# Optimization experiments

Measured on AMD Instinct MI355X. Metric: run time of the kernel, lower is better.

## Reference

```python
import jax, jax.numpy as jnp
import numpy as np

N, E, C, NB, NE, G = 20000, 320000, 64, 8, 4, 16
L2 = 9          # (max_ell+1)^2 with max_ell=2
RMAX = 5.0
HID = 16        # nonlinear readout hidden width


def setup_inputs():
    key = jax.random.key(0)
    ks = jax.random.split(key, 16)
    positions = jax.random.uniform(ks[0], (N, 3), dtype=jnp.float32) * 3.0
    elems = jax.random.randint(ks[1], (N,), 0, NE)
    node_attrs = jax.nn.one_hot(elems, NE, dtype=jnp.float32)
    edge_index = jax.random.randint(ks[2], (2, E), 0, N)
    batch = jnp.sort(jax.random.randint(ks[3], (N,), 0, G))
    shifts = jnp.zeros((E, 3), jnp.float32)
    atomic_energies = jnp.array([-1.0, -2.0, -3.0, -4.0], jnp.float32)
    sc = lambda k, shp, fan: jax.random.normal(k, shp, jnp.float32) / np.sqrt(fan).astype(np.float32)
    W_embed = sc(ks[4], (NE, C), NE)
    W_up = sc(ks[5], (2, C, C), C)
    W1 = sc(ks[6], (2, NB, 64), NB)
    W2 = sc(ks[7], (2, 64, C), 64)
    W_out = sc(ks[8], (2, C, C), C)
    W_skip = sc(ks[9], (2, NE, C), NE)
    w_read0 = sc(ks[10], (C,), C)
    W_r1 = sc(ks[11], (C, HID), C)
    w_r2 = sc(ks[12], (HID,), HID)
    return dict(positions=positions, node_attrs=node_attrs, shifts=shifts,
                atomic_energies=atomic_energies, W_embed=W_embed, W_up=W_up,
                W1=W1, W2=W2, W_out=W_out, W_skip=W_skip, w_read0=w_read0,
                W_r1=W_r1, w_r2=w_r2, edge_index=edge_index, batch=batch)


def _sph_harm_l2(u):
    # component-normalized real spherical harmonics up to l=2 on unit vectors
    x, y, z = u[:, 0], u[:, 1], u[:, 2]
    s3, s5, s15 = jnp.sqrt(3.0), jnp.sqrt(5.0), jnp.sqrt(15.0)
    return jnp.stack([jnp.ones_like(x),
                      s3 * x, s3 * y, s3 * z,
                      s15 * x * y, s15 * y * z, 0.5 * s5 * (3.0 * z * z - 1.0),
                      s15 * x * z, 0.5 * s15 * (x * x - y * y)], axis=-1)


def _radial(r):
    # Bessel radial basis with polynomial cutoff (p=6)
    n = jnp.arange(1, NB + 1, dtype=jnp.float32)
    rb = jnp.sqrt(2.0 / RMAX) * jnp.sin(n * jnp.pi * r[:, None] / RMAX) / r[:, None]
    u = r / RMAX
    fc = 1.0 - 28.0 * u**6 + 48.0 * u**7 - 21.0 * u**8
    fc = jnp.where(u < 1.0, fc, 0.0)
    return rb * fc[:, None]


def _energy_contributions(positions, node_attrs, shifts, atomic_energies,
                          W_embed, W_up, W1, W2, W_out, W_skip,
                          w_read0, W_r1, w_r2, edge_index, batch):
    snd, rcv = edge_index[0], edge_index[1]
    vec = positions[snd] - positions[rcv] + shifts                  # [E,3]
    r = jnp.sqrt(jnp.sum(vec * vec, axis=-1) + 1e-12)               # [E]
    Y = _sph_harm_l2(vec / r[:, None])                              # [E,L2]
    ef = _radial(r)                                                 # [E,NB]
    # E0: per-element reference energies, summed per graph
    e0 = jax.ops.segment_sum(node_attrs @ atomic_energies, batch, num_segments=G)
    h0 = node_attrs @ W_embed                                       # [N,C] scalar feats
    h = jnp.zeros((positions.shape[0], L2, C), h0.dtype).at[:, 0, :].set(h0)
    readouts = [lambda s: s @ w_read0,
                lambda s: jax.nn.silu(s @ W_r1) @ w_r2]             # linear / nonlinear
    energies = [e0]
    for i in range(2):
        hu = jnp.einsum('nlc,cd->nld', h, W_up[i])                  # channel mix
        R = jax.nn.silu(ef @ W1[i]) @ W2[i]                         # radial MLP [E,C]
        s = jnp.einsum('elc,el->ec', hu[snd], Y)                    # equivariant contraction
        m = Y[:, :, None] * (R * s)[:, None, :]                     # [E,L2,C] messages
        agg = jax.ops.segment_sum(m, rcv, num_segments=positions.shape[0])
        h = jnp.einsum('nlc,cd->nld', agg, W_out[i])
        h = h.at[:, 0, :].add(node_attrs @ W_skip[i])               # scalar skip connection
        node_en = readouts[i](h[:, 0, :])                           # [N]
        energies.append(jax.ops.segment_sum(node_en, batch, num_segments=G))
    return jnp.stack(energies, axis=-1)                             # [G, num_interactions+1]


def reference(positions, node_attrs, shifts, atomic_energies, W_embed, W_up,
              W1, W2, W_out, W_skip, w_read0, W_r1, w_r2, edge_index, batch):
    contributions = _energy_contributions(positions, node_attrs, shifts,
        atomic_energies, W_embed, W_up, W1, W2, W_out, W_skip,
        w_read0, W_r1, w_r2, edge_index, batch)
    total_energy = jnp.sum(contributions, axis=-1)                  # [G]
    forces = -jax.grad(lambda p: jnp.sum(_energy_contributions(p, node_attrs,
        shifts, atomic_energies, W_embed, W_up, W1, W2, W_out, W_skip,
        w_read0, W_r1, w_r2, edge_index, batch)))(positions)        # [N,3]
    return total_energy, contributions, forces
```

## Files before the change

kernel.cpp:

```cpp
#include <hip/hip_runtime.h>
#include <cmath>

constexpr int N_  = 20000;
constexpr int E_  = 320000;
constexpr int NE_ = 4;
constexpr int G_  = 16;
constexpr int CAP = 96;
constexpr int TAB = 4096;
constexpr float RMAXF = 5.0f;
constexpr float PI_F  = 3.14159265358979323846f;
constexpr float S3  = 1.7320508075688772f;
constexpr float S5  = 2.2360679774997896f;
constexpr float S15 = 3.8729833462074170f;
constexpr float KC_ = 0.6324555320336759f;

typedef unsigned short u16;
typedef unsigned int   u32;
typedef _Float16 f16;
typedef _Float16 f16x2 __attribute__((ext_vector_type(2)));

#define DEV static __device__ __forceinline__

__device__ float g_fallback[110000000];

DEV float sigmoidf_(float x){ return 1.0f/(1.0f+__expf(-x)); }

DEV float b2f(u16 u){ return __uint_as_float(((u32)u)<<16); }
DEV u16  f2b(float f){
  u32 x = __float_as_uint(f);
  return (u16)((x + 0x7FFFu + ((x>>16)&1u)) >> 16);
}
DEV u16  f2h(float f){ union{f16 h; u16 u;} v; v.h=(f16)f; return v.u; }
DEV float h2f(u16 u){ union{u16 u2; f16 h;} v; v.u2=u; return (float)v.h; }

DEV f16x2 u2h(u32 x){ union{u32 u; f16x2 h;} v; v.u=x; return v.h; }
DEV u32 h2u(f16x2 h){ union{u32 u; f16x2 h;} v; v.h=h; return v.u; }
DEV u32 pkh(float a, float b){ f16x2 h; h.x=(f16)a; h.y=(f16)b; return h2u(h); }

DEV void ld4(const float* __restrict__ p, float* d){
  float4 a = ((const float4*)p)[0];
  d[0]=a.x; d[1]=a.y; d[2]=a.z; d[3]=a.w;
}
DEV void ld4b(const u16* __restrict__ p, float* d){
  ushort4 a = *(const ushort4*)p;
  d[0]=b2f(a.x); d[1]=b2f(a.y); d[2]=b2f(a.z); d[3]=b2f(a.w);
}
DEV void st8h(u16* p, const float* d){
  uint4 v;
  v.x = pkh(d[0],d[1]); v.y = pkh(d[2],d[3]);
  v.z = pkh(d[4],d[5]); v.w = pkh(d[6],d[7]);
  *(uint4*)p = v;
}
DEV void ldY(const u16* __restrict__ p, float* Yb){
  ushort4 a = *(const ushort4*)p;
  ushort4 b = *(const ushort4*)(p+4);
  Yb[0]=h2f(a.x); Yb[1]=h2f(a.y); Yb[2]=h2f(a.z); Yb[3]=h2f(a.w);
  Yb[4]=h2f(b.x); Yb[5]=h2f(b.y); Yb[6]=h2f(b.z); Yb[7]=h2f(b.w);
}

DEV float tlerp(const u16* __restrict__ tab, int i0, float f, int idx){
  return h2f(tab[i0*256+idx])*(1.0f-f) + h2f(tab[(i0+1)*256+idx])*f;
}

__global__ void k_cnt(const int* __restrict__ ei, int* __restrict__ cntR){
  int e = blockIdx.x*256 + threadIdx.x;
  atomicAdd(&cntR[ei[E_+e]], 1);
}

__global__ void k_scan(const int* __restrict__ cntR, int* __restrict__ offR){
  __shared__ int part[256];
  int t = threadIdx.x;
  constexpr int CH = (N_+255)/256;
  int base = t*CH;
  int s=0;
  for (int i=0;i<CH;++i){ int idx=base+i; if(idx<N_) s+=cntR[idx]; }
  part[t]=s; __syncthreads();
  for (int d=1; d<256; d<<=1){
    int v = (t>=d)? part[t-d] : 0;
    __syncthreads();
    part[t]+=v;
    __syncthreads();
  }
  int run = (t==0)?0:part[t-1];
  for (int i=0;i<CH;++i){ int idx=base+i; if(idx<N_){ offR[idx]=run; run+=cntR[idx]; } }
  if (t==255) offR[N_]=run;
}

__global__ void k_perm(const int* __restrict__ ei, const int* __restrict__ offR,
                       int* __restrict__ cntR2, int* __restrict__ cntS,
                       int* __restrict__ pe, int* __restrict__ pSnd, int* __restrict__ pRcv,
                       int* __restrict__ listS){
  int e = blockIdx.x*256 + threadIdx.x;
  int s = ei[e], r = ei[E_+e];
  int p = offR[r] + atomicAdd(&cntR2[r], 1);
  pe[p] = e; pSnd[p] = s; pRcv[p] = r;
  int q = atomicAdd(&cntS[s], 1); if (q < CAP) listS[s*CAP+q] = p;
}

__global__ void k_pre(const float* __restrict__ Wout0, const float* __restrict__ Wup1,
                      const float* __restrict__ Wskip0, const float* __restrict__ wread0,
                      const float* __restrict__ Wemb, const float* __restrict__ Wup0,
                      float* __restrict__ WA, float* __restrict__ sa,
                      float* __restrict__ va, float* __restrict__ sv,
                      float* __restrict__ WembUp){
  int t = threadIdx.x;
  for (int idx=t; idx<4096; idx+=256){
    int c = idx>>6, d = idx&63;
    float acc=0.f;
    for (int m=0;m<64;++m) acc += Wout0[c*64+m]*Wup1[m*64+d];
    WA[idx]=acc;
  }
  {
    int k = t>>6, d = t&63;
    float acc=0.f;
    for (int m=0;m<64;++m) acc += Wskip0[k*64+m]*Wup1[m*64+d];
    sa[t]=acc;
    float acc2=0.f;
    for (int j=0;j<64;++j) acc2 += Wemb[k*64+j]*Wup0[j*64+d];
    WembUp[t]=acc2;
  }
  if (t<64){
    float acc=0.f;
    for (int d=0;d<64;++d) acc += Wout0[t*64+d]*wread0[d];
    va[t]=acc;
  }
  if (t<4){
    float acc=0.f;
    for (int d=0;d<64;++d) acc += Wskip0[t*64+d]*wread0[d];
    sv[t]=acc;
  }
}

__global__ __launch_bounds__(256, 2)
void k_rtab(const float* __restrict__ W1g, const float* __restrict__ W2g,
            u16* __restrict__ tab){
  __shared__ float sW1[1024];
  __shared__ u32   sW2h[4096];
  __shared__ u32   sAh[32*36];
  int t = threadIdx.x;
  for (int i=t;i<1024;i+=256) sW1[i]=W1g[i];
  for (int i=t;i<4096;i+=256){
    int L = i>>11, rem = i&2047, kp = rem>>6, c = rem&63;
    sW2h[i] = pkh(W2g[L*4096 + (2*kp)*64 + c], W2g[L*4096 + (2*kp+1)*64 + c]);
  }
  __syncthreads();
  int wid=t>>6, lane=t&63, q=lane>>3, j=lane&7, c0=j*8;
  int slot = wid*8 + q;
  int knot = blockIdx.x*32 + slot;
  bool valid = (knot <= TAB);
  float rad = fmaxf((float)knot * (RMAXF/(float)TAB), 1e-6f);
  float inv = 1.0f/rad;
  float tt = rad*(1.0f/RMAXF);
  float fc = 0.0f, dfc = 0.0f;
  if (tt < 1.0f){
    float t2=tt*tt, t4=t2*t2, t5=t4*tt, t6=t5*tt, t7=t6*tt, t8=t7*tt;
    fc  = 1.0f - 28.0f*t6 + 48.0f*t7 - 21.0f*t8;
    dfc = (-168.0f*t5 + 336.0f*t6 - 168.0f*t7)*(1.0f/RMAXF);
  }
  float th = rad*(PI_F/RMAXF);
  float s1 = __sinf(th), c1 = __cosf(th);
  float base = KC_*inv*fc;
  float efv[8], gfv[8];
  {
    float sb = s1, cb = c1;
    #pragma unroll
    for (int b=0;b<8;++b){
      efv[b] = base*sb;
      float wb_ = (float)(b+1)*(PI_F/RMAXF);
      float rb  = KC_*sb*inv;
      float drb = KC_*(wb_*cb - sb*inv)*inv;
      gfv[b] = drb*fc + rb*dfc;
      float sn = sb*c1 + cb*s1;
      cb = cb*c1 - sb*s1;
      sb = sn;
    }
  }
  u32* myAh = sAh + slot*36;
  for (int L=0; L<2; ++L){
    const float* w1 = sW1 + L*512;
    const u32*  w2h = sW2h + L*2048;
    float zz[8]={0,0,0,0,0,0,0,0};
    float wgv[8]={0,0,0,0,0,0,0,0};
    #pragma unroll 4
    for (int b=0;b<8;++b){
      float efb = efv[b], gfb = gfv[b];
      const float4* w=(const float4*)(w1 + b*64 + c0);
      float4 wa=w[0], wb=w[1];
      zz[0]+=efb*wa.x; zz[1]+=efb*wa.y; zz[2]+=efb*wa.z; zz[3]+=efb*wa.w;
      zz[4]+=efb*wb.x; zz[5]+=efb*wb.y; zz[6]+=efb*wb.z; zz[7]+=efb*wb.w;
      wgv[0]+=gfb*wa.x; wgv[1]+=gfb*wa.y; wgv[2]+=gfb*wa.z; wgv[3]+=gfb*wa.w;
      wgv[4]+=gfb*wb.x; wgv[5]+=gfb*wb.y; wgv[6]+=gfb*wb.z; wgv[7]+=gfb*wb.w;
    }
    float a[8], dv[8];
    #pragma unroll
    for (int i=0;i<8;++i){
      float sg = sigmoidf_(zz[i]);
      a[i]  = zz[i]*sg;
      float sp = sg*(1.0f + zz[i]*(1.0f - sg));
      dv[i] = wgv[i]*sp;
    }
    {
      uint4 av;
      av.x = pkh(a[0],a[1]); av.y = pkh(a[2],a[3]);
      av.z = pkh(a[4],a[5]); av.w = pkh(a[6],a[7]);
      *(uint4*)(myAh + 4*j) = av;
    }
    {
      float r0=0.f,r1=0.f,r2=0.f,r3=0.f,r4=0.f,r5=0.f,r6=0.f,r7=0.f;
      #pragma unroll 2
      for (int kp4=0; kp4<8; ++kp4){
        uint4 dq = *(const uint4*)(myAh + 4*kp4);
        #pragma unroll
        for (int i=0;i<4;++i){
          u32 du = (i==0)?dq.x:(i==1)?dq.y:(i==2)?dq.z:dq.w;
          f16x2 dh = u2h(du);
          const u32* wrow = w2h + (4*kp4+i)*64 + c0;
          uint4 w0 = *(const uint4*)(wrow);
          uint4 w1v = *(const uint4*)(wrow+4);
          r0 = __builtin_amdgcn_fdot2(dh, u2h(w0.x),  r0, false);
          r1 = __builtin_amdgcn_fdot2(dh, u2h(w0.y),  r1, false);
          r2 = __builtin_amdgcn_fdot2(dh, u2h(w0.z),  r2, false);
          r3 = __builtin_amdgcn_fdot2(dh, u2h(w0.w),  r3, false);
          r4 = __builtin_amdgcn_fdot2(dh, u2h(w1v.x), r4, false);
          r5 = __builtin_amdgcn_fdot2(dh, u2h(w1v.y), r5, false);
          r6 = __builtin_amdgcn_fdot2(dh, u2h(w1v.z), r6, false);
          r7 = __builtin_amdgcn_fdot2(dh, u2h(w1v.w), r7, false);
        }
      }
      float racc[8] = {r0,r1,r2,r3,r4,r5,r6,r7};
      if (valid) st8h(tab + (size_t)knot*256 + L*64 + c0, racc);
    }
    {
      uint4 av;
      av.x = pkh(dv[0],dv[1]); av.y = pkh(dv[2],dv[3]);
      av.z = pkh(dv[4],dv[5]); av.w = pkh(dv[6],dv[7]);
      *(uint4*)(myAh + 4*j) = av;
    }
    {
      float r0=0.f,r1=0.f,r2=0.f,r3=0.f,r4=0.f,r5=0.f,r6=0.f,r7=0.f;
      #pragma unroll 2
      for (int kp4=0; kp4<8; ++kp4){
        uint4 dq = *(const uint4*)(myAh + 4*kp4);
        #pragma unroll
        for (int i=0;i<4;++i){
          u32 du = (i==0)?dq.x:(i==1)?dq.y:(i==2)?dq.z:dq.w;
          f16x2 dh = u2h(du);
          const u32* wrow = w2h + (4*kp4+i)*64 + c0;
          uint4 w0 = *(const uint4*)(wrow);
          uint4 w1v = *(const uint4*)(wrow+4);
          r0 = __builtin_amdgcn_fdot2(dh, u2h(w0.x),  r0, false);
          r1 = __builtin_amdgcn_fdot2(dh, u2h(w0.y),  r1, false);
          r2 = __builtin_amdgcn_fdot2(dh, u2h(w0.z),  r2, false);
          r3 = __builtin_amdgcn_fdot2(dh, u2h(w0.w),  r3, false);
          r4 = __builtin_amdgcn_fdot2(dh, u2h(w1v.x), r4, false);
          r5 = __builtin_amdgcn_fdot2(dh, u2h(w1v.y), r5, false);
          r6 = __builtin_amdgcn_fdot2(dh, u2h(w1v.z), r6, false);
          r7 = __builtin_amdgcn_fdot2(dh, u2h(w1v.w), r7, false);
        }
      }
      float qacc[8] = {r0,r1,r2,r3,r4,r5,r6,r7};
      if (valid) st8h(tab + (size_t)knot*256 + 128 + L*64 + c0, qacc);
    }
  }
}

__global__ void k_fwd_edge(const float* __restrict__ pos, const float* __restrict__ shifts,
                const int* __restrict__ pe, const int* __restrict__ pSnd,
                const int* __restrict__ pRcv,
                u16* __restrict__ Y, float* __restrict__ u3,
                float* __restrict__ irr, float* __restrict__ xi){
  int e = blockIdx.x*256 + threadIdx.x;
  int eo  = pe[e];
  int snd = pSnd[e], rcv = pRcv[e];
  float vx = pos[snd*3+0]-pos[rcv*3+0]+shifts[(size_t)eo*3+0];
  float vy = pos[snd*3+1]-pos[rcv*3+1]+shifts[(size_t)eo*3+1];
  float vz = pos[snd*3+2]-pos[rcv*3+2]+shifts[(size_t)eo*3+2];
  float ss = vx*vx+vy*vy+vz*vz + 1e-12f;
  float rad = sqrtf(ss);
  float inv = 1.0f/rad;
  float x = vx*inv, y = vy*inv, z = vz*inv;
  irr[e]=inv;
  xi[e] = rad * ((float)TAB/RMAXF);
  u3[(size_t)e*3+0]=x; u3[(size_t)e*3+1]=y; u3[(size_t)e*3+2]=z;
  float Yf[8];
  Yf[0]=S3*x; Yf[1]=S3*y; Yf[2]=S3*z;
  Yf[3]=S15*x*y; Yf[4]=S15*y*z;
  Yf[5]=0.5f*S5*(3.0f*z*z-1.0f);
  Yf[6]=S15*x*z;
  Yf[7]=0.5f*S15*(x*x-y*y);
  st8h(Y + (size_t)e*8, Yf);
}

__global__ void k_e0(const float* __restrict__ attrs, const float* __restrict__ ae,
                     const int* __restrict__ batch, float* __restrict__ out){
  __shared__ float bins[G_];
  int t = threadIdx.x;
  if (t < G_) bins[t] = 0.f;
  __syncthreads();
  int n = blockIdx.x*256 + t;
  if (n < N_){
    float v = 0.f;
    #pragma unroll
    for (int k=0;k<NE_;++k) v += attrs[n*NE_+k]*ae[k];
    atomicAdd(&bins[batch[n]], v);
  }
  __syncthreads();
  if (t < G_){
    float b = bins[t];
    if (b != 0.f){
      atomicAdd(&out[t], b);
      atomicAdd(&out[G_ + t*3 + 0], b);
    }
  }
}

__global__ void k_hu0(const float* __restrict__ attrs, const float* __restrict__ WembUp,
                      float* __restrict__ hu0){
  int i = blockIdx.x*256 + threadIdx.x;
  int n = i>>6, c = i&63;
  float acc = 0.f;
  #pragma unroll
  for (int k=0;k<NE_;++k) acc += attrs[n*NE_+k]*WembUp[k*64+c];
  hu0[i] = acc;
}

__global__ void k_agg0(const int* __restrict__ offR, const int* __restrict__ pSnd,
                       const float* __restrict__ hu0,
                       const u16* __restrict__ tab, const float* __restrict__ xi,
                       const u16* __restrict__ Y,
                       u16* __restrict__ agg0){
  int t = threadIdx.x; int n = blockIdx.x*4 + (t>>6); int c = t&63;
  float acc[9] = {0,0,0,0,0,0,0,0,0};
  int p0 = offR[n], p1 = offR[n+1];
  for (int p=p0;p<p1;++p){
    int s = pSnd[p];
    float xiv = xi[p];
    float r0v = 0.f;
    if (xiv < (float)TAB){
      int i0 = (int)xiv; float f = xiv - (float)i0;
      r0v = tlerp(tab, i0, f, c);
    }
    float v = r0v*hu0[(size_t)s*64+c];
    float Yb[8];
    ldY(Y + (size_t)p*8, Yb);
    acc[0] += v;
    #pragma unroll
    for (int l=1;l<9;++l) acc[l] += Yb[l-1]*v;
  }
  #pragma unroll
  for (int l=0;l<9;++l) agg0[((size_t)n*9+l)*64+c] = f2h(acc[l]);
}

__global__ void k_s1(const int* __restrict__ cntS, const int* __restrict__ listS,
                     const u16* __restrict__ hu1, const u16* __restrict__ Y,
                     u16* __restrict__ s1){
  int t = threadIdx.x; int n = blockIdx.x*4 + (t>>6); int c = t&63;
  float hu[9];
  #pragma unroll
  for (int l=0;l<9;++l) hu[l] = b2f(hu1[((size_t)n*9+l)*64+c]);
  int deg = min(cntS[n], CAP);
  #pragma unroll 2
  for (int j=0;j<deg;++j){
    int p = listS[n*CAP+j];
    float Yb[8];
    ldY(Y + (size_t)p*8, Yb);
    float acc = hu[0];
    #pragma unroll
    for (int l=1;l<9;++l) acc += hu[l]*Yb[l-1];
    s1[(size_t)p*64+c] = f2h(acc);
  }
}

__global__ void k_agg1(const int* __restrict__ offR,
                       const u16* __restrict__ tab, const float* __restrict__ xi,
                       const u16* __restrict__ s1,
                       float* __restrict__ agg1){
  int t = threadIdx.x; int n = blockIdx.x*4 + (t>>6); int c = t&63;
  float acc = 0.f;
  int p0 = offR[n], p1 = offR[n+1];
  for (int p=p0;p<p1;++p){
    float xiv = xi[p];
    float r1v = 0.f;
    if (xiv < (float)TAB){
      int i0 = (int)xiv; float f = xiv - (float)i0;
      r1v = tlerp(tab, i0, f, 64 + c);
    }
    acc += r1v*h2f(s1[(size_t)p*64+c]);
  }
  agg1[(size_t)n*64+c] = acc;
}

__global__ void k_dhu1(const int* __restrict__ cntS, const int* __restrict__ listS,
                       const int* __restrict__ pRcv,
                       const u16* __restrict__ tab, const float* __restrict__ xi,
                       const float* __restrict__ ga1, const u16* __restrict__ Y,
                       u16* __restrict__ dhu1){
  int t = threadIdx.x; int n = blockIdx.x*4 + (t>>6); int c = t&63;
  float acc[9] = {0,0,0,0,0,0,0,0,0};
  int deg = min(cntS[n], CAP);
  #pragma unroll 2
  for (int j=0;j<deg;++j){
    int p = listS[n*CAP+j];
    int r = pRcv[p];
    float xiv = xi[p];
    float r1v = 0.f;
    if (xiv < (float)TAB){
      int i0 = (int)xiv; float f = xiv - (float)i0;
      r1v = tlerp(tab, i0, f, 64 + c);
    }
    float ds = r1v*ga1[(size_t)r*64+c];
    float Yb[8];
    ldY(Y + (size_t)p*8, Yb);
    acc[0] += ds;
    #pragma unroll
    for (int l=1;l<9;++l) acc[l] += Yb[l-1]*ds;
  }
  #pragma unroll
  for (int l=0;l<9;++l) dhu1[((size_t)n*9+l)*64+c] = f2h(acc[l]);
}

template<bool TRANS, bool OUTB, bool IN16>
__global__ __launch_bounds__(256, 2)
void k_mm64(const void* __restrict__ in, const float* __restrict__ W,
            void* __restrict__ out, int rows, int lper,
            const float* __restrict__ attrs, const float* __restrict__ Wsk,
            const float* __restrict__ bias){
  __shared__ float sWT[64*68];
  __shared__ float sRow[4*68];
  int t = threadIdx.x;
  for (int i=t;i<4096;i+=256){
    int k=i&63, c=i>>6;
    sWT[c*68+k] = TRANS ? W[c*64+k] : W[k*64+c];
  }
  __syncthreads();
  int wid = t>>6, c = t&63;
  float wcol[64];
  {
    const float4* wp = (const float4*)(sWT + c*68);
    #pragma unroll
    for (int kk=0;kk<16;++kk){
      float4 w4 = wp[kk];
      wcol[4*kk+0]=w4.x; wcol[4*kk+1]=w4.y; wcol[4*kk+2]=w4.z; wcol[4*kk+3]=w4.w;
    }
  }
  float* myRow = sRow + wid*68;
  for (int it=0; it<8; ++it){
    int row = (blockIdx.x*8+it)*4 + wid;
    if (IN16) myRow[c] = h2f(((const u16*)in)[(size_t)row*64+c]);
    else      myRow[c] = ((const float*)in)[(size_t)row*64+c];
    float acc = 0.f;
    #pragma unroll
    for (int kk=0;kk<16;++kk){
      float4 r4 = ((const float4*)myRow)[kk];
      acc += r4.x*wcol[4*kk+0] + r4.y*wcol[4*kk+1] + r4.z*wcol[4*kk+2] + r4.w*wcol[4*kk+3];
    }
    if (lper==1 || (row % 9)==0){
      int n = (lper==1) ? row : (row/9);
      if (attrs){
        #pragma unroll
        for (int k=0;k<NE_;++k) acc += attrs[n*NE_+k]*Wsk[k*64+c];
      }
      if (bias) acc += bias[c];
    }
    if (OUTB) ((u16*)out)[(size_t)row*64+c] = f2b(acc);
    else      ((float*)out)[(size_t)row*64+c] = acc;
  }
}

__global__ void k_read0(const u16* __restrict__ agg0, const float* __restrict__ va,
                        const float* __restrict__ sv, const float* __restrict__ attrs,
                        const int* __restrict__ batch, float* __restrict__ out){
  __shared__ float bins[G_];
  int t = threadIdx.x;
  if (t < G_) bins[t] = 0.f;
  __syncthreads();
  int lane = t & 63, wid = t >> 6;
  int grp = lane >> 3, j = lane & 7;
  int n = blockIdx.x*32 + wid*8 + grp;
  const u16* hp = agg0 + (size_t)n*576 + j*8;
  float h[8];
  ldY(hp, h);
  const float* wp = va + j*8;
  float4 w0v = ((const float4*)wp)[0], w4v = ((const float4*)wp)[1];
  float v = h[0]*w0v.x + h[1]*w0v.y + h[2]*w0v.z + h[3]*w0v.w
          + h[4]*w4v.x + h[5]*w4v.y + h[6]*w4v.z + h[7]*w4v.w;
  v += __shfl_xor(v,1,64); v += __shfl_xor(v,2,64); v += __shfl_xor(v,4,64);
  if (j==0){
    v += attrs[n*NE_+0]*sv[0] + attrs[n*NE_+1]*sv[1]
       + attrs[n*NE_+2]*sv[2] + attrs[n*NE_+3]*sv[3];
    atomicAdd(&bins[batch[n]], v);
  }
  __syncthreads();
  if (t < G_){
    float b = bins[t];
    if (b != 0.f){
      atomicAdd(&out[t], b);
      atomicAdd(&out[G_ + t*3 + 1], b);
    }
  }
}

__global__ void k_read1(const float* __restrict__ h2, const float* __restrict__ Wr1,
                        const float* __restrict__ wr2, const int* __restrict__ batch,
                        float* __restrict__ spz, float* __restrict__ out){
  __shared__ float sW[64*16];
  __shared__ float sA[256];
  __shared__ float bins[G_];
  int t = threadIdx.x;
  for (int i=t;i<1024;i+=256) sW[i]=Wr1[i];
  if (t < G_) bins[t] = 0.f;
  __syncthreads();
  int n = blockIdx.x*16 + (t>>4); int j = t&15;
  float z = 0.f;
  #pragma unroll 16
  for (int c=0;c<64;++c) z += h2[(size_t)n*64+c]*sW[c*16+j];
  float sg = sigmoidf_(z);
  float a  = z*sg;
  float sp = sg*(1.0f + z*(1.0f - sg));
  float w2v = wr2[j];
  spz[n*16+j] = sp*w2v;
  sA[t] = a*w2v;
  __syncthreads();
  if (j==0){
    float s = 0.f;
    #pragma unroll
    for (int k=0;k<16;++k) s += sA[t+k];
    atomicAdd(&bins[batch[n]], s);
  }
  __syncthreads();
  if (t < G_){
    float b = bins[t];
    if (b != 0.f){
      atomicAdd(&out[t], b);
      atomicAdd(&out[G_ + t*3 + 2], b);
    }
  }
}

__global__ void k_dh2(const float* __restrict__ Wr1, const float* __restrict__ spz,
                      float* __restrict__ dh2){
  int i = blockIdx.x*256 + threadIdx.x;
  int n = i>>6, c = i&63;
  float acc = 0.f;
  #pragma unroll
  for (int j=0;j<16;++j) acc += Wr1[c*16+j]*spz[n*16+j];
  dh2[i] = acc;
}

__global__ __launch_bounds__(256, 4)
void k_bedge_all(const int* __restrict__ pSnd, const int* __restrict__ pRcv,
             const u16* __restrict__ Y,
             const float* __restrict__ u3, const float* __restrict__ irr,
             const u16* __restrict__ tab, const float* __restrict__ xi,
             const float* __restrict__ ga1, const u16* __restrict__ ga0,
             const float* __restrict__ hu0, const u16* __restrict__ hu1,
             float* __restrict__ gF){
  int t = threadIdx.x;
  int wid=t>>6, lane=t&63, q=lane>>4, j=lane&15, c0=j*4;
  int slot = wid*4+q;
  int e = blockIdx.x*16 + slot;
  int snd = pSnd[e], rcv = pRcv[e];
  float Yl[9];
  Yl[0]=1.0f;
  ldY(Y + (size_t)e*8, Yl+1);
  ushort4 huv1[9];
  #pragma unroll
  for (int l=0;l<9;++l) huv1[l] = *(const ushort4*)(hu1 + ((size_t)snd*9 + l)*64 + c0);
  ushort4 gv0[9];
  #pragma unroll
  for (int l=0;l<9;++l) gv0[l] = *(const ushort4*)(ga0 + ((size_t)rcv*9 + l)*64 + c0);
  float T1[4];  ld4(ga1 + (size_t)rcv*64 + c0, T1);
  float hu0v[4]; ld4(hu0 + (size_t)snd*64 + c0, hu0v);
  float xiv = xi[e];
  float R0v[4], R1v[4], q0v[4], q1v[4];
  if (xiv < (float)TAB){
    int i0 = (int)xiv; float f = xiv - (float)i0, g = 1.0f - f;
    const u16* ra = tab + (size_t)i0*256;
    const u16* rb = ra + 256;
    ushort4 a, b;
    a = *(const ushort4*)(ra + c0);        b = *(const ushort4*)(rb + c0);
    R0v[0]=h2f(a.x)*g+h2f(b.x)*f; R0v[1]=h2f(a.y)*g+h2f(b.y)*f;
    R0v[2]=h2f(a.z)*g+h2f(b.z)*f; R0v[3]=h2f(a.w)*g+h2f(b.w)*f;
    a = *(const ushort4*)(ra + 64 + c0);   b = *(const ushort4*)(rb + 64 + c0);
    R1v[0]=h2f(a.x)*g+h2f(b.x)*f; R1v[1]=h2f(a.y)*g+h2f(b.y)*f;
    R1v[2]=h2f(a.z)*g+h2f(b.z)*f; R1v[3]=h2f(a.w)*g+h2f(b.w)*f;
    a = *(const ushort4*)(ra + 128 + c0);  b = *(const ushort4*)(rb + 128 + c0);
    q0v[0]=h2f(a.x)*g+h2f(b.x)*f; q0v[1]=h2f(a.y)*g+h2f(b.y)*f;
    q0v[2]=h2f(a.z)*g+h2f(b.z)*f; q0v[3]=h2f(a.w)*g+h2f(b.w)*f;
    a = *(const ushort4*)(ra + 192 + c0);  b = *(const ushort4*)(rb + 192 + c0);
    q1v[0]=h2f(a.x)*g+h2f(b.x)*f; q1v[1]=h2f(a.y)*g+h2f(b.y)*f;
    q1v[2]=h2f(a.z)*g+h2f(b.z)*f; q1v[3]=h2f(a.w)*g+h2f(b.w)*f;
  } else {
    #pragma unroll
    for (int i=0;i<4;++i){ R0v[i]=0.f; R1v[i]=0.f; q0v[i]=0.f; q1v[i]=0.f; }
  }
  float dyp[9];
  float dR1[4];
  {
    float ds1[4], sA[4];
    #pragma unroll
    for (int i=0;i<4;++i){ ds1[i]=R1v[i]*T1[i]; sA[i]=0.f; }
    #pragma unroll
    for (int l=0;l<9;++l){
      float h0v=b2f(huv1[l].x), h1v=b2f(huv1[l].y), h2v=b2f(huv1[l].z), h3v=b2f(huv1[l].w);
      float Ylv = Yl[l];
      sA[0]+=h0v*Ylv; sA[1]+=h1v*Ylv; sA[2]+=h2v*Ylv; sA[3]+=h3v*Ylv;
      dyp[l] = ds1[0]*h0v + ds1[1]*h1v + ds1[2]*h2v + ds1[3]*h3v;
    }
    #pragma unroll
    for (int i=0;i<4;++i) dR1[i]=sA[i]*T1[i];
  }
  float dR0[4];
  {
    float P[4], T0[4];
    #pragma unroll
    for (int i=0;i<4;++i){ P[i]=R0v[i]*hu0v[i]; T0[i]=0.f; }
    #pragma unroll
    for (int l=0;l<9;++l){
      float g0=b2f(gv0[l].x), g1=b2f(gv0[l].y), g2=b2f(gv0[l].z), g3=b2f(gv0[l].w);
      float Ylv = Yl[l];
      T0[0]+=g0*Ylv; T0[1]+=g1*Ylv; T0[2]+=g2*Ylv; T0[3]+=g3*Ylv;
      dyp[l] += g0*P[0] + g1*P[1] + g2*P[2] + g3*P[3];
    }
    #pragma unroll
    for (int i=0;i<4;++i) dR0[i]=hu0v[i]*T0[i];
  }
  float dy[9];
  #pragma unroll
  for (int l=1;l<9;++l){
    float v=dyp[l];
    v += __shfl_xor(v,1,64); v += __shfl_xor(v,2,64);
    v += __shfl_xor(v,4,64); v += __shfl_xor(v,8,64);
    dy[l]=v;
  }
  float dr = q1v[0]*dR1[0]+q1v[1]*dR1[1]+q1v[2]*dR1[2]+q1v[3]*dR1[3]
           + q0v[0]*dR0[0]+q0v[1]*dR0[1]+q0v[2]*dR0[2]+q0v[3]*dR0[3];
  dr += __shfl_xor(dr,1,64); dr += __shfl_xor(dr,2,64);
  dr += __shfl_xor(dr,4,64); dr += __shfl_xor(dr,8,64);
  float x = u3[(size_t)e*3+0], y = u3[(size_t)e*3+1], zz = u3[(size_t)e*3+2];
  float invr = irr[e];
  float dux = S3*dy[1] + S15*(y*dy[4] + zz*dy[7] + x*dy[8]);
  float duy = S3*dy[2] + S15*(x*dy[4] + zz*dy[5] - y*dy[8]);
  float duz = S3*dy[3] + S15*(y*dy[5] + x*dy[7]) + 3.0f*S5*zz*dy[6];
  float udot = x*dux + y*duy + zz*duz;
  float gx = dr*x + invr*(dux - x*udot);
  float gy = dr*y + invr*(duy - y*udot);
  float gz = dr*zz + invr*(duz - zz*udot);
  if (j==0){
    float* gp2 = gF + (size_t)e*3;
    gp2[0]=gx; gp2[1]=gy; gp2[2]=gz;
  }
}

__global__ void k_fsum(const int* __restrict__ offR, const int* __restrict__ cntS,
                       const int* __restrict__ listS,
                       const float* __restrict__ gF, float* __restrict__ F){
  int t = threadIdx.x;
  int lane = t & 63, wid = t >> 6;
  int sub = lane >> 3, j = lane & 7;
  int n = blockIdx.x*32 + wid*8 + sub;
  float fx=0.f, fy=0.f, fz=0.f;
  int p0 = offR[n], p1 = offR[n+1];
  for (int p=p0+j; p<p1; p+=8){
    fx += gF[(size_t)p*3+0]; fy += gF[(size_t)p*3+1]; fz += gF[(size_t)p*3+2];
  }
  int dSn = min(cntS[n], CAP);
  for (int k=j;k<dSn;k+=8){
    int p = listS[n*CAP+k];
    fx -= gF[(size_t)p*3+0]; fy -= gF[(size_t)p*3+1]; fz -= gF[(size_t)p*3+2];
  }
  fx += __shfl_xor(fx,1,64); fy += __shfl_xor(fy,1,64); fz += __shfl_xor(fz,1,64);
  fx += __shfl_xor(fx,2,64); fy += __shfl_xor(fy,2,64); fz += __shfl_xor(fz,2,64);
  fx += __shfl_xor(fx,4,64); fy += __shfl_xor(fy,4,64); fz += __shfl_xor(fz,4,64);
  if (j==0){
    F[n*3+0]=fx; F[n*3+1]=fy; F[n*3+2]=fz;
  }
}

extern "C" void kernel_launch(void* const* d_in, const int* in_sizes, int n_in,
                              void* d_out, int out_size, void* d_ws, size_t ws_size,
                              hipStream_t stream){
  (void)in_sizes; (void)n_in;
  const float* pos    = (const float*)d_in[0];
  const float* attrs  = (const float*)d_in[1];
  const float* shifts = (const float*)d_in[2];
  const float* ae     = (const float*)d_in[3];
  const float* Wemb   = (const float*)d_in[4];
  const float* Wup    = (const float*)d_in[5];
  const float* W1     = (const float*)d_in[6];
  const float* W2     = (const float*)d_in[7];
  const float* Wout   = (const float*)d_in[8];
  const float* Wskip  = (const float*)d_in[9];
  const float* wread0 = (const float*)d_in[10];
  const float* Wr1    = (const float*)d_in[11];
  const float* wr2    = (const float*)d_in[12];
  const int*   ei     = (const int*)d_in[13];
  const int*   batch  = (const int*)d_in[14];
  float* out = (float*)d_out;

  const size_t NEED = 430000000;
  char* base;
  if (ws_size >= NEED){
    base = (char*)d_ws;
  } else {
    void* p = nullptr;
    hipGetSymbolAddress(&p, HIP_SYMBOL(g_fallback));
    base = (char*)p;
  }
  size_t off = 0;
  auto alloc = [&](size_t bytes)->char*{
    char* p = base + off;
    off += ((bytes + 255)/256)*256;
    return p;
  };
  u16*   Y    = (u16*)  alloc((size_t)E_*8*2);
  float* u3   = (float*)alloc((size_t)E_*3*4);
  float* irr  = (float*)alloc((size_t)E_*4);
  float* xi   = (float*)alloc((size_t)E_*4);
  u16*   s1b  = (u16*)  alloc((size_t)E_*64*2);
  float* gF   = (float*)alloc((size_t)E_*3*4);
  u16*   tab  = (u16*)  alloc((size_t)(TAB+1)*256*2);
  float* hu0  = (float*)alloc((size_t)N_*64*4);
  u16*   hu1  = (u16*)  alloc((size_t)N_*9*64*2);
  u16*   agg0 = (u16*)  alloc((size_t)N_*9*64*2);
  float* agg1 = (float*)alloc((size_t)N_*64*4);
  float* h2   = (float*)alloc((size_t)N_*64*4);
  float* spz  = (float*)alloc((size_t)N_*16*4);
  float* dh2  = (float*)alloc((size_t)N_*64*4);
  float* ga1  = (float*)alloc((size_t)N_*64*4);
  u16*   ga0  = (u16*)  alloc((size_t)N_*9*64*2);
  float* WembUp = (float*)alloc(256*4);
  float* WA   = (float*)alloc(4096*4);
  float* sa   = (float*)alloc(256*4);
  float* va   = (float*)alloc(64*4);
  float* sv   = (float*)alloc(4*4);
  int* cnts  = (int*)alloc((size_t)3*N_*4);
  int* offR  = (int*)alloc((size_t)(N_+1)*4);
  int* pe    = (int*)alloc((size_t)E_*4);
  int* pSnd  = (int*)alloc((size_t)E_*4);
  int* pRcv  = (int*)alloc((size_t)E_*4);
  int* listS = (int*)alloc((size_t)N_*CAP*4);
  int* cntR = cnts;  int* cntS = cnts + N_;  int* cntR2 = cnts + 2*N_;
  u16* dhu1 = agg0;
  float* F = out + G_ + G_*3;

  hipMemsetAsync(d_out, 0, (size_t)out_size*sizeof(float), stream);
  hipMemsetAsync(cnts, 0, (size_t)3*N_*sizeof(int), stream);

  k_cnt     <<<E_/256, 256, 0, stream>>>(ei, cntR);
  k_scan    <<<1, 256, 0, stream>>>(cntR, offR);
  k_perm    <<<E_/256, 256, 0, stream>>>(ei, offR, cntR2, cntS, pe, pSnd, pRcv, listS);

  k_rtab    <<<(TAB+1+31)/32, 256, 0, stream>>>(W1, W2, tab);
  k_fwd_edge<<<E_/256, 256, 0, stream>>>(pos, shifts, pe, pSnd, pRcv, Y, u3, irr, xi);
  k_pre     <<<1, 256, 0, stream>>>(Wout, Wup + 4096, Wskip, wread0, Wemb, Wup, WA, sa, va, sv, WembUp);
  k_e0      <<<(N_+255)/256, 256, 0, stream>>>(attrs, ae, batch, out);
  k_hu0     <<<N_*64/256, 256, 0, stream>>>(attrs, WembUp, hu0);
  k_agg0    <<<N_/4, 256, 0, stream>>>(offR, pSnd, hu0, tab, xi, Y, agg0);
  k_mm64<false,true,true><<<N_*9/32, 256, 0, stream>>>(agg0, WA, hu1, N_*9, 9, attrs, sa, nullptr);
  k_read0   <<<N_/32, 256, 0, stream>>>(agg0, va, sv, attrs, batch, out);
  k_s1      <<<N_/4, 256, 0, stream>>>(cntS, listS, hu1, Y, s1b);
  k_agg1    <<<N_/4, 256, 0, stream>>>(offR, tab, xi, s1b, agg1);
  k_mm64<false,false,false><<<N_/32, 256, 0, stream>>>(agg1, Wout + 4096, h2, N_, 1, attrs, Wskip + 256, nullptr);
  k_read1   <<<N_/16, 256, 0, stream>>>(h2, Wr1, wr2, batch, spz, out);

  k_dh2     <<<N_*64/256, 256, 0, stream>>>(Wr1, spz, dh2);
  k_mm64<true,false,false><<<N_/32, 256, 0, stream>>>(dh2, Wout + 4096, ga1, N_, 1, nullptr, nullptr, nullptr);
  k_dhu1    <<<N_/4, 256, 0, stream>>>(cntS, listS, pRcv, tab, xi, ga1, Y, dhu1);
  k_mm64<true,true,true><<<N_*9/32, 256, 0, stream>>>(dhu1, WA, ga0, N_*9, 9, nullptr, nullptr, va);
  k_bedge_all<<<E_/16, 256, 0, stream>>>(pSnd, pRcv, Y, u3, irr, tab, xi, ga1, ga0, hu0, hu1, gF);
  k_fsum    <<<N_/32, 256, 0, stream>>>(offR, cntS, listS, gF, F);
}
```

Measured before the change: 751.8 us.

## Fuse small node kernels: recompute hu0 on the fly, fold e0 and dh2 chain

Removes the k_hu0, k_e0, k_dh2 kernels and one k_mm64 launch. hu0 is now recomputed from the one-hot attrs and WembUp wherever it is read (agg0, bedge). The e0 energy reduction is folded into k_read0. The ga1 backward path is precomputed as a 16x64 matrix CC = Wr1^T·Wout1^T and applied inside k_read1. This cuts launches and the hu0/dh2/spz global memory traffic, at the cost of a few extra FMAs per edge.

```diff
diff --git a/kernel.cpp b/kernel.cpp
--- a/kernel.cpp
+++ b/kernel.cpp
@@ -40,10 +40,6 @@
 DEV void ld4(const float* __restrict__ p, float* d){
   float4 a = ((const float4*)p)[0];
   d[0]=a.x; d[1]=a.y; d[2]=a.z; d[3]=a.w;
-}
-DEV void ld4b(const u16* __restrict__ p, float* d){
-  ushort4 a = *(const ushort4*)p;
-  d[0]=b2f(a.x); d[1]=b2f(a.y); d[2]=b2f(a.z); d[3]=b2f(a.w);
 }
 DEV void st8h(u16* p, const float* d){
   uint4 v;
@@ -100,9 +96,10 @@
 __global__ void k_pre(const float* __restrict__ Wout0, const float* __restrict__ Wup1,
                       const float* __restrict__ Wskip0, const float* __restrict__ wread0,
                       const float* __restrict__ Wemb, const float* __restrict__ Wup0,
+                      const float* __restrict__ Wr1, const float* __restrict__ Wout1,
                       float* __restrict__ WA, float* __restrict__ sa,
                       float* __restrict__ va, float* __restrict__ sv,
-                      float* __restrict__ WembUp){
+                      float* __restrict__ WembUp, float* __restrict__ CC){
   int t = threadIdx.x;
   for (int idx=t; idx<4096; idx+=256){
     int c = idx>>6, d = idx&63;
@@ -118,6 +115,12 @@
     float acc2=0.f;
     for (int j=0;j<64;++j) acc2 += Wemb[k*64+j]*Wup0[j*64+d];
     WembUp[t]=acc2;
+  }
+  for (int idx=t; idx<1024; idx+=256){
+    int j = idx>>6, c = idx&63;
+    float acc=0.f;
+    for (int k=0;k<64;++k) acc += Wr1[k*16+j]*Wout1[c*64+k];
+    CC[idx]=acc;
   }
   if (t<64){
     float acc=0.f;
@@ -291,45 +294,13 @@
   st8h(Y + (size_t)e*8, Yf);
 }
 
-__global__ void k_e0(const float* __restrict__ attrs, const float* __restrict__ ae,
-                     const int* __restrict__ batch, float* __restrict__ out){
-  __shared__ float bins[G_];
-  int t = threadIdx.x;
-  if (t < G_) bins[t] = 0.f;
-  __syncthreads();
-  int n = blockIdx.x*256 + t;
-  if (n < N_){
-    float v = 0.f;
-    #pragma unroll
-    for (int k=0;k<NE_;++k) v += attrs[n*NE_+k]*ae[k];
-    atomicAdd(&bins[batch[n]], v);
-  }
-  __syncthreads();
-  if (t < G_){
-    float b = bins[t];
-    if (b != 0.f){
-      atomicAdd(&out[t], b);
-      atomicAdd(&out[G_ + t*3 + 0], b);
-    }
-  }
-}
-
-__global__ void k_hu0(const float* __restrict__ attrs, const float* __restrict__ WembUp,
-                      float* __restrict__ hu0){
-  int i = blockIdx.x*256 + threadIdx.x;
-  int n = i>>6, c = i&63;
-  float acc = 0.f;
-  #pragma unroll
-  for (int k=0;k<NE_;++k) acc += attrs[n*NE_+k]*WembUp[k*64+c];
-  hu0[i] = acc;
-}
-
 __global__ void k_agg0(const int* __restrict__ offR, const int* __restrict__ pSnd,
-                       const float* __restrict__ hu0,
+                       const float* __restrict__ attrs, const float* __restrict__ WembUp,
                        const u16* __restrict__ tab, const float* __restrict__ xi,
                        const u16* __restrict__ Y,
                        u16* __restrict__ agg0){
   int t = threadIdx.x; int n = blockIdx.x*4 + (t>>6); int c = t&63;
+  float we0 = WembUp[0*64+c], we1 = WembUp[1*64+c], we2 = WembUp[2*64+c], we3 = WembUp[3*64+c];
   float acc[9] = {0,0,0,0,0,0,0,0,0};
   int p0 = offR[n], p1 = offR[n+1];
   for (int p=p0;p<p1;++p){
@@ -340,7 +311,9 @@
       int i0 = (int)xiv; float f = xiv - (float)i0;
       r0v = tlerp(tab, i0, f, c);
     }
-    float v = r0v*hu0[(size_t)s*64+c];
+    float4 av = *(const float4*)(attrs + (size_t)s*4);
+    float hu0c = av.x*we0 + av.y*we1 + av.z*we2 + av.w*we3;
+    float v = r0v*hu0c;
     float Yb[8];
     ldY(Y + (size_t)p*8, Yb);
     acc[0] += v;
@@ -469,10 +442,12 @@
 
 __global__ void k_read0(const u16* __restrict__ agg0, const float* __restrict__ va,
                         const float* __restrict__ sv, const float* __restrict__ attrs,
+                        const float* __restrict__ ae,
                         const int* __restrict__ batch, float* __restrict__ out){
-  __shared__ float bins[G_];
+  __shared__ float bins0[G_];
+  __shared__ float bins1[G_];
   int t = threadIdx.x;
-  if (t < G_) bins[t] = 0.f;
+  if (t < G_){ bins0[t] = 0.f; bins1[t] = 0.f; }
   __syncthreads();
   int lane = t & 63, wid = t >> 6;
   int grp = lane >> 3, j = lane & 7;
@@ -486,31 +461,39 @@
           + h[4]*w4v.x + h[5]*w4v.y + h[6]*w4v.z + h[7]*w4v.w;
   v += __shfl_xor(v,1,64); v += __shfl_xor(v,2,64); v += __shfl_xor(v,4,64);
   if (j==0){
-    v += attrs[n*NE_+0]*sv[0] + attrs[n*NE_+1]*sv[1]
-       + attrs[n*NE_+2]*sv[2] + attrs[n*NE_+3]*sv[3];
-    atomicAdd(&bins[batch[n]], v);
+    float4 av = *(const float4*)(attrs + (size_t)n*4);
+    v += av.x*sv[0] + av.y*sv[1] + av.z*sv[2] + av.w*sv[3];
+    float e0v = av.x*ae[0] + av.y*ae[1] + av.z*ae[2] + av.w*ae[3];
+    int b = batch[n];
+    atomicAdd(&bins1[b], v);
+    atomicAdd(&bins0[b], e0v);
   }
   __syncthreads();
   if (t < G_){
-    float b = bins[t];
-    if (b != 0.f){
-      atomicAdd(&out[t], b);
-      atomicAdd(&out[G_ + t*3 + 1], b);
+    float b0 = bins0[t], b1 = bins1[t];
+    if (b0 != 0.f || b1 != 0.f){
+      atomicAdd(&out[t], b0 + b1);
+      if (b0 != 0.f) atomicAdd(&out[G_ + t*3 + 0], b0);
+      if (b1 != 0.f) atomicAdd(&out[G_ + t*3 + 1], b1);
     }
   }
 }
 
 __global__ void k_read1(const float* __restrict__ h2, const float* __restrict__ Wr1,
                         const float* __restrict__ wr2, const int* __restrict__ batch,
-                        float* __restrict__ spz, float* __restrict__ out){
+                        const float* __restrict__ CC,
+                        float* __restrict__ ga1, float* __restrict__ out){
   __shared__ float sW[64*16];
+  __shared__ float sCC[16*64];
+  __shared__ float sSp[256];
   __shared__ float sA[256];
   __shared__ float bins[G_];
   int t = threadIdx.x;
-  for (int i=t;i<1024;i+=256) sW[i]=Wr1[i];
+  for (int i=t;i<1024;i+=256){ sW[i]=Wr1[i]; sCC[i]=CC[i]; }
   if (t < G_) bins[t] = 0.f;
   __syncthreads();
-  int n = blockIdx.x*16 + (t>>4); int j = t&15;
+  int nn = t>>4; int j = t&15;
+  int n = blockIdx.x*16 + nn;
   float z = 0.f;
   #pragma unroll 16
   for (int c=0;c<64;++c) z += h2[(size_t)n*64+c]*sW[c*16+j];
@@ -518,13 +501,25 @@
   float a  = z*sg;
   float sp = sg*(1.0f + z*(1.0f - sg));
   float w2v = wr2[j];
-  spz[n*16+j] = sp*w2v;
-  sA[t] = a*w2v;
+  sSp[t] = sp*w2v;
+  sA[t]  = a*w2v;
   __syncthreads();
+  {
+    int cb = j*4;
+    float g0=0.f,g1=0.f,g2=0.f,g3=0.f;
+    const float* sp_ = sSp + nn*16;
+    #pragma unroll
+    for (int jp=0;jp<16;++jp){
+      float s = sp_[jp];
+      const float* cc = sCC + jp*64 + cb;
+      g0 += s*cc[0]; g1 += s*cc[1]; g2 += s*cc[2]; g3 += s*cc[3];
+    }
+    *(float4*)(ga1 + (size_t)n*64 + cb) = make_float4(g0,g1,g2,g3);
+  }
   if (j==0){
     float s = 0.f;
     #pragma unroll
-    for (int k=0;k<16;++k) s += sA[t+k];
+    for (int k=0;k<16;++k) s += sA[nn*16+k];
     atomicAdd(&bins[batch[n]], s);
   }
   __syncthreads();
@@ -537,29 +532,26 @@
   }
 }
 
-__global__ void k_dh2(const float* __restrict__ Wr1, const float* __restrict__ spz,
-                      float* __restrict__ dh2){
-  int i = blockIdx.x*256 + threadIdx.x;
-  int n = i>>6, c = i&63;
-  float acc = 0.f;
-  #pragma unroll
-  for (int j=0;j<16;++j) acc += Wr1[c*16+j]*spz[n*16+j];
-  dh2[i] = acc;
-}
-
 __global__ __launch_bounds__(256, 4)
 void k_bedge_all(const int* __restrict__ pSnd, const int* __restrict__ pRcv,
              const u16* __restrict__ Y,
              const float* __restrict__ u3, const float* __restrict__ irr,
              const u16* __restrict__ tab, const float* __restrict__ xi,
              const float* __restrict__ ga1, const u16* __restrict__ ga0,
-             const float* __restrict__ hu0, const u16* __restrict__ hu1,
+             const float* __restrict__ attrs, const float* __restrict__ WembUp,
+             const u16* __restrict__ hu1,
              float* __restrict__ gF){
   int t = threadIdx.x;
   int wid=t>>6, lane=t&63, q=lane>>4, j=lane&15, c0=j*4;
   int slot = wid*4+q;
   int e = blockIdx.x*16 + slot;
   int snd = pSnd[e], rcv = pRcv[e];
+  float wembr[4][4];
+  #pragma unroll
+  for (int k=0;k<4;++k){
+    float4 wr = *(const float4*)(WembUp + k*64 + c0);
+    wembr[k][0]=wr.x; wembr[k][1]=wr.y; wembr[k][2]=wr.z; wembr[k][3]=wr.w;
+  }
   float Yl[9];
   Yl[0]=1.0f;
   ldY(Y + (size_t)e*8, Yl+1);
@@ -570,7 +562,11 @@
   #pragma unroll
   for (int l=0;l<9;++l) gv0[l] = *(const ushort4*)(ga0 + ((size_t)rcv*9 + l)*64 + c0);
   float T1[4];  ld4(ga1 + (size_t)rcv*64 + c0, T1);
-  float hu0v[4]; ld4(hu0 + (size_t)snd*64 + c0, hu0v);
+  float4 av = *(const float4*)(attrs + (size_t)snd*4);
+  float hu0v[4];
+  #pragma unroll
+  for (int i=0;i<4;++i)
+    hu0v[i] = av.x*wembr[0][i] + av.y*wembr[1][i] + av.z*wembr[2][i] + av.w*wembr[3][i];
   float xiv = xi[e];
   float R0v[4], R1v[4], q0v[4], q1v[4];
   if (xiv < (float)TAB){
@@ -720,13 +716,10 @@
   u16*   s1b  = (u16*)  alloc((size_t)E_*64*2);
   float* gF   = (float*)alloc((size_t)E_*3*4);
   u16*   tab  = (u16*)  alloc((size_t)(TAB+1)*256*2);
-  float* hu0  = (float*)alloc((size_t)N_*64*4);
   u16*   hu1  = (u16*)  alloc((size_t)N_*9*64*2);
   u16*   agg0 = (u16*)  alloc((size_t)N_*9*64*2);
   float* agg1 = (float*)alloc((size_t)N_*64*4);
   float* h2   = (float*)alloc((size_t)N_*64*4);
-  float* spz  = (float*)alloc((size_t)N_*16*4);
-  float* dh2  = (float*)alloc((size_t)N_*64*4);
   float* ga1  = (float*)alloc((size_t)N_*64*4);
   u16*   ga0  = (u16*)  alloc((size_t)N_*9*64*2);
   float* WembUp = (float*)alloc(256*4);
@@ -734,6 +727,7 @@
   float* sa   = (float*)alloc(256*4);
   float* va   = (float*)alloc(64*4);
   float* sv   = (float*)alloc(4*4);
+  float* CC   = (float*)alloc(1024*4);
   int* cnts  = (int*)alloc((size_t)3*N_*4);
   int* offR  = (int*)alloc((size_t)(N_+1)*4);
   int* pe    = (int*)alloc((size_t)E_*4);
@@ -753,21 +747,17 @@
 
   k_rtab    <<<(TAB+1+31)/32, 256, 0, stream>>>(W1, W2, tab);
   k_fwd_edge<<<E_/256, 256, 0, stream>>>(pos, shifts, pe, pSnd, pRcv, Y, u3, irr, xi);
-  k_pre     <<<1, 256, 0, stream>>>(Wout, Wup + 4096, Wskip, wread0, Wemb, Wup, WA, sa, va, sv, WembUp);
-  k_e0      <<<(N_+255)/256, 256, 0, stream>>>(attrs, ae, batch, out);
-  k_hu0     <<<N_*64/256, 256, 0, stream>>>(attrs, WembUp, hu0);
-  k_agg0    <<<N_/4, 256, 0, stream>>>(offR, pSnd, hu0, tab, xi, Y, agg0);
+  k_pre     <<<1, 256, 0, stream>>>(Wout, Wup + 4096, Wskip, wread0, Wemb, Wup, Wr1, Wout + 4096, WA, sa, va, sv, WembUp, CC);
+  k_agg0    <<<N_/4, 256, 0, stream>>>(offR, pSnd, attrs, WembUp, tab, xi, Y, agg0);
   k_mm64<false,true,true><<<N_*9/32, 256, 0, stream>>>(agg0, WA, hu1, N_*9, 9, attrs, sa, nullptr);
-  k_read0   <<<N_/32, 256, 0, stream>>>(agg0, va, sv, attrs, batch, out);
+  k_read0   <<<N_/32, 256, 0, stream>>>(agg0, va, sv, attrs, ae, batch, out);
   k_s1      <<<N_/4, 256, 0, stream>>>(cntS, listS, hu1, Y, s1b);
   k_agg1    <<<N_/4, 256, 0, stream>>>(offR, tab, xi, s1b, agg1);
   k_mm64<false,false,false><<<N_/32, 256, 0, stream>>>(agg1, Wout + 4096, h2, N_, 1, attrs, Wskip + 256, nullptr);
-  k_read1   <<<N_/16, 256, 0, stream>>>(h2, Wr1, wr2, batch, spz, out);
-
-  k_dh2     <<<N_*64/256, 256, 0, stream>>>(Wr1, spz, dh2);
-  k_mm64<true,false,false><<<N_/32, 256, 0, stream>>>(dh2, Wout + 4096, ga1, N_, 1, nullptr, nullptr, nullptr);
+  k_read1   <<<N_/16, 256, 0, stream>>>(h2, Wr1, wr2, batch, CC, ga1, out);
+
   k_dhu1    <<<N_/4, 256, 0, stream>>>(cntS, listS, pRcv, tab, xi, ga1, Y, dhu1);
   k_mm64<true,true,true><<<N_*9/32, 256, 0, stream>>>(dhu1, WA, ga0, N_*9, 9, nullptr, nullptr, va);
-  k_bedge_all<<<E_/16, 256, 0, stream>>>(pSnd, pRcv, Y, u3, irr, tab, xi, ga1, ga0, hu0, hu1, gF);
+  k_bedge_all<<<E_/16, 256, 0, stream>>>(pSnd, pRcv, Y, u3, irr, tab, xi, ga1, ga0, attrs, WembUp, hu1, gF);
   k_fsum    <<<N_/32, 256, 0, stream>>>(offR, cntS, listS, gF, F);
 }
```

Result: faster. 727.6 us (-3.2%).
